# Kernel tuning notes

Hardware: AMD Instinct MI355X
Metric: run time of the kernel (lower is better)

Reference implementation:

```python
import jax, jax.numpy as jnp
import numpy as np

N_EMBD = 128
N_HEADS = 8
HEAD_SIZE = N_EMBD // N_HEADS  # 16
EPS = 1e-5


def _layernorm(x, g, b):
    m = jnp.mean(x, axis=-1, keepdims=True)
    v = jnp.mean(jnp.square(x - m), axis=-1, keepdims=True)
    return (x - m) * jax.lax.rsqrt(v + EPS) * g + b


def setup_inputs() -> dict:
    key = jax.random.key(0)
    ks = jax.random.split(key, 12)
    B, T, D, H, HS = 16, 1024, N_EMBD, N_HEADS, HEAD_SIZE
    s = 1.0 / np.sqrt(D)
    inp = {
        "x": jax.random.normal(ks[0], (B, T, D), jnp.float32),
        # per-head QKV projections (stacked over heads; matches ModuleList of Linear(D, HS))
        "Wq": jax.random.uniform(ks[1], (H, D, HS), jnp.float32, -s, s),
        "bq": jnp.zeros((H, HS), jnp.float32),
        "Wk": jax.random.uniform(ks[2], (H, D, HS), jnp.float32, -s, s),
        "bk": jnp.zeros((H, HS), jnp.float32),
        "Wv": jax.random.uniform(ks[3], (H, D, HS), jnp.float32, -s, s),
        "bv": jnp.zeros((H, HS), jnp.float32),
        "Wp": jax.random.uniform(ks[4], (H * HS, D), jnp.float32, -s, s),
        "bp": jnp.zeros((D,), jnp.float32),
        "W1": jax.random.uniform(ks[5], (D, 4 * D), jnp.float32, -s, s),
        "b1": jnp.zeros((4 * D,), jnp.float32),
        "W2": jax.random.uniform(ks[6], (4 * D, D), jnp.float32, -1.0 / np.sqrt(4 * D), 1.0 / np.sqrt(4 * D)),
        "b2": jnp.zeros((D,), jnp.float32),
        "g1": jnp.ones((D,), jnp.float32),
        "be1": jnp.zeros((D,), jnp.float32),
        "g2": jnp.ones((D,), jnp.float32),
        "be2": jnp.zeros((D,), jnp.float32),
    }
    return inp


def reference(x, Wq, bq, Wk, bk, Wv, bv, Wp, bp, W1, b1, W2, b2, g1, be1, g2, be2):
    B, T, D = x.shape
    # batched per-head projections: [B,T,D] x [H,D,HS] -> [B,H,T,HS]
    q = jnp.einsum("btd,hds->bhts", x, Wq) + bq[None, :, None, :]
    k = jnp.einsum("btd,hds->bhts", x, Wk) + bk[None, :, None, :]
    v = jnp.einsum("btd,hds->bhts", x, Wv) + bv[None, :, None, :]
    scores = jnp.einsum("bhts,bhus->bhtu", q, k) / np.sqrt(HEAD_SIZE).astype(np.float32)
    tril = jnp.tril(jnp.ones((T, T), x.dtype))
    # faithful to source: multiplicative + additive mask (not -inf where)
    scores = scores * tril - 1e12 * (1.0 - tril)
    attn = jax.nn.softmax(scores, axis=-1)
    out = jnp.einsum("bhtu,bhus->bhts", attn, v)  # [B,H,T,HS]
    # concat heads in head order -> [B,T,H*HS]
    out = out.transpose(0, 2, 1, 3).reshape(B, T, -1)
    attn_out = out @ Wp + bp
    x = _layernorm(attn_out + x, g1, be1)
    h = jax.nn.gelu(x @ W1 + b1, approximate=False) @ W2 + b2
    x = _layernorm(h + x, g2, be2)
    return x
```

## Files before the change

### kernel.cpp

```cpp
#include <hip/hip_runtime.h>
#include <hip/hip_bf16.h>
#include <math.h>

constexpr int NB  = 16;
constexpr int NT  = 1024;
constexpr int ND  = 128;
constexpr int NH  = 8;
constexpr int NHS = 16;
constexpr int NDH = 512;
constexpr long NBT = (long)NB * NT;

typedef __attribute__((ext_vector_type(8))) short short8;
typedef __attribute__((ext_vector_type(4))) float f32x4;
typedef __attribute__((ext_vector_type(16))) float f32x16;
typedef __attribute__((ext_vector_type(4))) unsigned short us4;

__device__ __forceinline__ unsigned short f2bf(float f) {
    __hip_bfloat16 h = __float2bfloat16(f);
    return *(unsigned short*)&h;
}

__device__ __forceinline__ short8 cvt8(const float* p) {
    const float4 f0 = *(const float4*)p;
    const float4 f1 = *(const float4*)(p + 4);
    union { short8 s; __hip_bfloat162 h[4]; } u;
    u.h[0] = __float22bfloat162_rn(make_float2(f0.x, f0.y));
    u.h[1] = __float22bfloat162_rn(make_float2(f0.z, f0.w));
    u.h[2] = __float22bfloat162_rn(make_float2(f1.x, f1.y));
    u.h[3] = __float22bfloat162_rn(make_float2(f1.z, f1.w));
    return u.s;
}

__device__ __forceinline__ float fast_gelu(float y) {
    const float t = y * y;
    const float u = __builtin_fmaf(y * 0.044715f, t, y);
    const float e = __builtin_amdgcn_exp2f(u * -2.302118131f);
    return y * __builtin_amdgcn_rcpf(1.0f + e);
}

__global__ __launch_bounds__(256) void k_prep(
    const float* __restrict__ Wq, const float* __restrict__ Wk,
    const float* __restrict__ Wv, __hip_bfloat16* __restrict__ Wqkvt)
{
    const int blk = blockIdx.x, tid = threadIdx.x;
    const int i0 = blk * 1024 + tid * 4;
    const int n = i0 >> 7, d0 = i0 & 127;
    const int sec = n >> 7, m = n & 127;
    const float* W = (sec == 0) ? Wq : (sec == 1) ? Wk : Wv;
    const float* src = W + (m >> 4) * 2048 + (m & 15);
    us4 v;
    #pragma unroll
    for (int j = 0; j < 4; ++j) v[j] = f2bf(src[(d0 + j) * 16]);
    *(us4*)((unsigned short*)Wqkvt + i0) = v;
}

__global__ __launch_bounds__(256) void k_qkv(
    const float* __restrict__ x, const __hip_bfloat16* __restrict__ Wqkvt,
    const float* __restrict__ bq, const float* __restrict__ bk,
    const float* __restrict__ bv,
    const float* __restrict__ Wp, const float* __restrict__ W1,
    const float* __restrict__ W2,
    __hip_bfloat16* __restrict__ Wpt, __hip_bfloat16* __restrict__ W1t,
    __hip_bfloat16* __restrict__ W2t,
    __hip_bfloat16* __restrict__ qo, __hip_bfloat16* __restrict__ ko,
    __hip_bfloat16* __restrict__ vo)
{
    __shared__ __align__(16) unsigned short st[32 * 392];
    const int tid = threadIdx.x;

    if (blockIdx.x >= 512) {
        const int blk = blockIdx.x - 512 + 48;
        us4 v;
        if (blk < 64) {
            const int i0 = (blk - 48) * 1024 + tid * 4;
            const int n = i0 >> 7, d0 = i0 & 127;
            #pragma unroll
            for (int j = 0; j < 4; ++j) v[j] = f2bf(Wp[(d0 + j) * 128 + n]);
            *(us4*)((unsigned short*)Wpt + i0) = v;
        } else if (blk < 128) {
            const int i0 = (blk - 64) * 1024 + tid * 4;
            const int n = i0 >> 7, d0 = i0 & 127;
            #pragma unroll
            for (int j = 0; j < 4; ++j) v[j] = f2bf(W1[(d0 + j) * 512 + n]);
            *(us4*)((unsigned short*)W1t + i0) = v;
        } else {
            const int i0 = (blk - 128) * 1024 + tid * 4;
            const int n = i0 >> 9, k0 = i0 & 511;
            #pragma unroll
            for (int j = 0; j < 4; ++j) v[j] = f2bf(W2[(k0 + j) * 128 + n]);
            *(us4*)((unsigned short*)W2t + i0) = v;
        }
        return;
    }

    const int w    = tid >> 6;
    const int lane = tid & 63;
    const int sL   = lane & 15;
    const int quad = lane >> 4;
    const int tok0 = blockIdx.x * 32;

    const unsigned short* W = (const unsigned short*)Wqkvt;

    short8 bx[2][4];
    #pragma unroll
    for (int tt = 0; tt < 2; ++tt)
        #pragma unroll
        for (int ks = 0; ks < 4; ++ks)
            bx[tt][ks] = cvt8(x + (size_t)(tok0 + tt * 16 + sL) * 128 + ks * 32 + quad * 8);

    f32x4 acc[6][2];
    #pragma unroll
    for (int ci = 0; ci < 6; ++ci)
        #pragma unroll
        for (int tt = 0; tt < 2; ++tt)
            acc[ci][tt] = (f32x4){0.f, 0.f, 0.f, 0.f};

    #pragma unroll
    for (int ks = 0; ks < 4; ++ks) {
        short8 aW[6];
        #pragma unroll
        for (int ci = 0; ci < 6; ++ci) {
            const int ct = w * 6 + ci;
            aW[ci] = *(const short8*)(W + (size_t)(ct * 16 + sL) * 128 + ks * 32 + quad * 8);
        }
        #pragma unroll
        for (int ci = 0; ci < 6; ++ci)
            #pragma unroll
            for (int tt = 0; tt < 2; ++tt)
                acc[ci][tt] = __builtin_amdgcn_mfma_f32_16x16x32_bf16(aW[ci], bx[tt][ks], acc[ci][tt], 0, 0, 0);
    }

    const float qscale = 0.3606737602f;
    #pragma unroll
    for (int ci = 0; ci < 6; ++ci) {
        const int ct = w * 6 + ci;
        const int kind = ct >> 3;
        const int ncc = (ct & 7) * 16 + quad * 4;
        const float4 bb = *(const float4*)(((kind == 0) ? bq : (kind == 1) ? bk : bv) + ncc);
        #pragma unroll
        for (int tt = 0; tt < 2; ++tt) {
            us4 v;
            #pragma unroll
            for (int r = 0; r < 4; ++r) {
                float val = acc[ci][tt][r] + ((const float*)&bb)[r];
                if (kind == 0) val *= qscale;
                v[r] = f2bf(val);
            }
            *(us4*)(st + (tt * 16 + sL) * 392 + ct * 16 + quad * 4) = v;
        }
    }
    __syncthreads();

    const int b = tok0 >> 10, tt0 = tok0 & 1023;
    {
        const int h = tid >> 5, tok = tid & 31;
        const unsigned short* sq = st + tok * 392 + h * 16;
        const unsigned short* sk = st + tok * 392 + 128 + h * 16;
        unsigned short* dq = (unsigned short*)qo + ((size_t)(b * 8 + h) * 1024 + tt0 + tok) * 16;
        unsigned short* dk = (unsigned short*)ko + ((size_t)(b * 8 + h) * 1024 + tt0 + tok) * 16;
        *(short8*)dq       = *(const short8*)sq;
        *(short8*)(dq + 8) = *(const short8*)(sq + 8);
        *(short8*)dk       = *(const short8*)sk;
        *(short8*)(dk + 8) = *(const short8*)(sk + 8);
    }
    if (tid < 128) {
        const int h = tid >> 4, s = tid & 15;
        unsigned short tmp[32];
        #pragma unroll
        for (int tok = 0; tok < 32; ++tok)
            tmp[tok] = st[tok * 392 + 256 + h * 16 + s];
        unsigned short* dv = (unsigned short*)vo + ((size_t)(b * 8 + h) * 16 + s) * 1024 + tt0;
        #pragma unroll
        for (int j = 0; j < 4; ++j)
            *(short8*)(dv + j * 8) = *(const short8*)(tmp + j * 8);
    }
}

__global__ __launch_bounds__(256) void k_attn(
    const __hip_bfloat16* __restrict__ qb, const __hip_bfloat16* __restrict__ kb,
    const __hip_bfloat16* __restrict__ vtb, __hip_bfloat16* __restrict__ att)
{
    __shared__ __align__(16) float stg[4][32 * 16];
    const int bh   = blockIdx.x & 127;
    const int sub  = blockIdx.x >> 7;
    const int wave = threadIdx.x >> 6;
    const int lane = threadIdx.x & 63;
    const int col  = lane & 31;
    const int hi   = lane >> 5;
    const int b = bh >> 3, h = bh & 7;
    const int tile = sub * 4 + wave;
    const int t0 = tile * 32;

    const unsigned short* qp = (const unsigned short*)qb  + (size_t)bh * NT * NHS;
    const unsigned short* kp = (const unsigned short*)kb  + (size_t)bh * NT * NHS;
    const unsigned short* vp = (const unsigned short*)vtb + (size_t)bh * NHS * NT;

    const short8 bQ = *(const short8*)(qp + (size_t)(t0 + col) * NHS + hi * 8);
    const unsigned short* vrow = vp + (size_t)(col & 15) * NT + hi * 8;

    f32x16 o;
    #pragma unroll
    for (int r = 0; r < 16; ++r) o[r] = 0.f;
    f32x16 zc;
    #pragma unroll
    for (int r = 0; r < 16; ++r) zc[r] = 0.f;
    float lp0 = 0.f, lp1 = 0.f, lp2 = 0.f, lp3 = 0.f;

    for (int c = 0; c <= tile; ++c) {
        const int u0 = c * 32;
        const short8 aK  = *(const short8*)(kp + (size_t)(u0 + col) * NHS + hi * 8);
        const short8 bV0 = *(const short8*)(vrow + u0);
        const short8 bV1 = *(const short8*)(vrow + u0 + 16);

        const f32x16 sT = __builtin_amdgcn_mfma_f32_32x32x16_bf16(aK, bQ, zc, 0, 0, 0);

        float p[16];
        if (c < tile) {
            #pragma unroll
            for (int r = 0; r < 16; ++r) p[r] = __builtin_amdgcn_exp2f(sT[r]);
        } else {
            const int kh = 4 * hi;
            #pragma unroll
            for (int r = 0; r < 16; ++r) {
                const int kc = (r & 3) + 8 * (r >> 2) + kh;
                const float e = __builtin_amdgcn_exp2f(sT[r]);
                p[r] = (kc <= col) ? e : 0.f;
            }
        }
        #pragma unroll
        for (int r = 0; r < 16; r += 4) {
            lp0 += p[r]; lp1 += p[r + 1]; lp2 += p[r + 2]; lp3 += p[r + 3];
        }

        int d[8];
        #pragma unroll
        for (int i = 0; i < 8; ++i) {
            __hip_bfloat162 hh = __float22bfloat162_rn(make_float2(p[2 * i], p[2 * i + 1]));
            d[i] = *(int*)&hh;
        }
        auto s0 = __builtin_amdgcn_permlane32_swap(d[0], d[2], false, false);
        auto s1 = __builtin_amdgcn_permlane32_swap(d[1], d[3], false, false);
        auto s2 = __builtin_amdgcn_permlane32_swap(d[4], d[6], false, false);
        auto s3 = __builtin_amdgcn_permlane32_swap(d[5], d[7], false, false);
        union { int i[4]; short8 v; } A0, A1;
        A0.i[0] = s0[0]; A0.i[1] = s1[0]; A0.i[2] = s0[1]; A0.i[3] = s1[1];
        A1.i[0] = s2[0]; A1.i[1] = s3[0]; A1.i[2] = s2[1]; A1.i[3] = s3[1];

        o = __builtin_amdgcn_mfma_f32_32x32x16_bf16(A0.v, bV0, o, 0, 0, 0);
        o = __builtin_amdgcn_mfma_f32_32x32x16_bf16(A1.v, bV1, o, 0, 0, 0);
    }

    float lp = (lp0 + lp1) + (lp2 + lp3);
    lp += __shfl_xor(lp, 32);
    const float inv = 1.0f / lp;

    float* sp = stg[wave];
    if (col < 16) {
        #pragma unroll
        for (int r = 0; r < 16; ++r) {
            const int qr = (r & 3) + 8 * (r >> 2) + 4 * hi;
            sp[qr * 16 + col] = o[r];
        }
    }
    __syncthreads();
    const float invq = __shfl(inv, lane >> 1);
    const float* rp = sp + (lane >> 1) * 16 + (lane & 1) * 8;
    const float4 va = *(const float4*)rp;
    const float4 vb = *(const float4*)(rp + 4);
    union { short8 v; unsigned short u[8]; } res;
    res.u[0] = f2bf(va.x * invq); res.u[1] = f2bf(va.y * invq);
    res.u[2] = f2bf(va.z * invq); res.u[3] = f2bf(va.w * invq);
    res.u[4] = f2bf(vb.x * invq); res.u[5] = f2bf(vb.y * invq);
    res.u[6] = f2bf(vb.z * invq); res.u[7] = f2bf(vb.w * invq);
    unsigned short* dst = (unsigned short*)att +
        ((size_t)b * NT + t0 + (lane >> 1)) * ND + h * NHS + (lane & 1) * 8;
    *(short8*)dst = res.v;
}

__global__ __launch_bounds__(256) void k_tail(
    const __hip_bfloat16* __restrict__ attb, const __hip_bfloat16* __restrict__ Wpt,
    const __hip_bfloat16* __restrict__ W1t, const __hip_bfloat16* __restrict__ W2t,
    const float* __restrict__ x, const float* __restrict__ bp,
    const float* __restrict__ g1, const float* __restrict__ be1,
    const float* __restrict__ b1, const float* __restrict__ b2,
    const float* __restrict__ g2, const float* __restrict__ be2,
    float* __restrict__ out)
{
    __shared__ float ys[32][132];
    __shared__ __align__(16) unsigned short l1b[32 * 136];
    __shared__ __align__(16) unsigned short midb[32 * 528];
    const int w    = threadIdx.x >> 6;
    const int lane = threadIdx.x & 63;
    const int sL   = lane & 15;
    const int quad = lane >> 4;
    const int tok0 = blockIdx.x * 32;

    {
        const unsigned short* A = (const unsigned short*)attb;
        const unsigned short* W = (const unsigned short*)Wpt;
        short8 bfr[2][4];
        #pragma unroll
        for (int tt = 0; tt < 2; ++tt)
            #pragma unroll
            for (int ks = 0; ks < 4; ++ks)
                bfr[tt][ks] = *(const short8*)(A + (size_t)(tok0 + tt * 16 + sL) * 128 + ks * 32 + quad * 8);

        f32x4 acc[2][2];
        #pragma unroll
        for (int ci = 0; ci < 2; ++ci)
            #pragma unroll
            for (int tt = 0; tt < 2; ++tt)
                acc[ci][tt] = (f32x4){0.f, 0.f, 0.f, 0.f};

        #pragma unroll
        for (int ks = 0; ks < 4; ++ks) {
            short8 aW[2];
            #pragma unroll
            for (int ci = 0; ci < 2; ++ci)
                aW[ci] = *(const short8*)(W + (size_t)((w * 2 + ci) * 16 + sL) * 128 + ks * 32 + quad * 8);
            #pragma unroll
            for (int ci = 0; ci < 2; ++ci)
                #pragma unroll
                for (int tt = 0; tt < 2; ++tt)
                    acc[ci][tt] = __builtin_amdgcn_mfma_f32_16x16x32_bf16(aW[ci], bfr[tt][ks], acc[ci][tt], 0, 0, 0);
        }
        #pragma unroll
        for (int ci = 0; ci < 2; ++ci) {
            const int n0 = (w * 2 + ci) * 16 + quad * 4;
            const float4 bb = *(const float4*)(bp + n0);
            #pragma unroll
            for (int tt = 0; tt < 2; ++tt) {
                float4 v;
                v.x = acc[ci][tt][0] + bb.x; v.y = acc[ci][tt][1] + bb.y;
                v.z = acc[ci][tt][2] + bb.z; v.w = acc[ci][tt][3] + bb.w;
                *(float4*)(&ys[tt * 16 + sL][n0]) = v;
            }
        }
    }
    __syncthreads();

    const int tok = threadIdx.x >> 3;
    const int l8  = threadIdx.x & 7;
    const int c0  = l8 * 16;
    {
        float vals[16];
        float s = 0.f, s2 = 0.f;
        #pragma unroll
        for (int ch = 0; ch < 4; ++ch) {
            const float4 ly = *(const float4*)&ys[tok][c0 + ch * 4];
            const float4 gx = *(const float4*)(x + (size_t)(tok0 + tok) * 128 + c0 + ch * 4);
            vals[ch*4+0] = ly.x + gx.x; vals[ch*4+1] = ly.y + gx.y;
            vals[ch*4+2] = ly.z + gx.z; vals[ch*4+3] = ly.w + gx.w;
            #pragma unroll
            for (int j = 0; j < 4; ++j) { s += vals[ch*4+j]; s2 += vals[ch*4+j] * vals[ch*4+j]; }
        }
        #pragma unroll
        for (int off = 1; off <= 4; off <<= 1) {
            s  += __shfl_xor(s, off, 8);
            s2 += __shfl_xor(s2, off, 8);
        }
        const float mean = s * (1.0f / 128.0f);
        const float var  = s2 * (1.0f / 128.0f) - mean * mean;
        const float rstd = rsqrtf(var + 1e-5f);
        #pragma unroll
        for (int ch = 0; ch < 4; ++ch) {
            const float4 gg = *(const float4*)(g1 + c0 + ch * 4);
            const float4 bb = *(const float4*)(be1 + c0 + ch * 4);
            float ln0 = (vals[ch*4+0] - mean) * rstd * gg.x + bb.x;
            float ln1v = (vals[ch*4+1] - mean) * rstd * gg.y + bb.y;
            float ln2v = (vals[ch*4+2] - mean) * rstd * gg.z + bb.z;
            float ln3 = (vals[ch*4+3] - mean) * rstd * gg.w + bb.w;
            ys[tok][c0 + ch*4 + 0] = ln0;
            ys[tok][c0 + ch*4 + 1] = ln1v;
            ys[tok][c0 + ch*4 + 2] = ln2v;
            ys[tok][c0 + ch*4 + 3] = ln3;
            us4 lb;
            lb[0] = f2bf(ln0); lb[1] = f2bf(ln1v); lb[2] = f2bf(ln2v); lb[3] = f2bf(ln3);
            *(us4*)(l1b + tok * 136 + c0 + ch * 4) = lb;
        }
    }
    __syncthreads();

    {
        const unsigned short* W = (const unsigned short*)W1t;
        short8 bl[2][4];
        #pragma unroll
        for (int tt = 0; tt < 2; ++tt)
            #pragma unroll
            for (int ks = 0; ks < 4; ++ks)
                bl[tt][ks] = *(const short8*)(l1b + (tt * 16 + sL) * 136 + ks * 32 + quad * 8);

        f32x4 acc[8][2];
        #pragma unroll
        for (int ci = 0; ci < 8; ++ci)
            #pragma unroll
            for (int tt = 0; tt < 2; ++tt)
                acc[ci][tt] = (f32x4){0.f, 0.f, 0.f, 0.f};

        #pragma unroll
        for (int ks = 0; ks < 4; ++ks) {
            short8 aW[8];
            #pragma unroll
            for (int ci = 0; ci < 8; ++ci)
                aW[ci] = *(const short8*)(W + (size_t)((w * 8 + ci) * 16 + sL) * 128 + ks * 32 + quad * 8);
            #pragma unroll
            for (int ci = 0; ci < 8; ++ci)
                #pragma unroll
                for (int tt = 0; tt < 2; ++tt)
                    acc[ci][tt] = __builtin_amdgcn_mfma_f32_16x16x32_bf16(aW[ci], bl[tt][ks], acc[ci][tt], 0, 0, 0);
        }
        #pragma unroll
        for (int ci = 0; ci < 8; ++ci) {
            const int n0 = (w * 8 + ci) * 16 + quad * 4;
            const float4 bb = *(const float4*)(b1 + n0);
            #pragma unroll
            for (int tt = 0; tt < 2; ++tt) {
                us4 v;
                v[0] = f2bf(fast_gelu(acc[ci][tt][0] + bb.x));
                v[1] = f2bf(fast_gelu(acc[ci][tt][1] + bb.y));
                v[2] = f2bf(fast_gelu(acc[ci][tt][2] + bb.z));
                v[3] = f2bf(fast_gelu(acc[ci][tt][3] + bb.w));
                *(us4*)(midb + (tt * 16 + sL) * 528 + n0) = v;
            }
        }
    }
    __syncthreads();

    f32x4 acc2[2][2];
    #pragma unroll
    for (int ci = 0; ci < 2; ++ci)
        #pragma unroll
        for (int tt = 0; tt < 2; ++tt)
            acc2[ci][tt] = (f32x4){0.f, 0.f, 0.f, 0.f};
    {
        const unsigned short* W = (const unsigned short*)W2t;
        #pragma unroll
        for (int ks = 0; ks < 16; ++ks) {
            short8 bm0 = *(const short8*)(midb + (size_t)sL * 528 + ks * 32 + quad * 8);
            short8 bm1 = *(const short8*)(midb + (size_t)(16 + sL) * 528 + ks * 32 + quad * 8);
            short8 aW0 = *(const short8*)(W + (size_t)((w * 2) * 16 + sL) * 512 + ks * 32 + quad * 8);
            short8 aW1 = *(const short8*)(W + (size_t)((w * 2 + 1) * 16 + sL) * 512 + ks * 32 + quad * 8);
            acc2[0][0] = __builtin_amdgcn_mfma_f32_16x16x32_bf16(aW0, bm0, acc2[0][0], 0, 0, 0);
            acc2[0][1] = __builtin_amdgcn_mfma_f32_16x16x32_bf16(aW0, bm1, acc2[0][1], 0, 0, 0);
            acc2[1][0] = __builtin_amdgcn_mfma_f32_16x16x32_bf16(aW1, bm0, acc2[1][0], 0, 0, 0);
            acc2[1][1] = __builtin_amdgcn_mfma_f32_16x16x32_bf16(aW1, bm1, acc2[1][1], 0, 0, 0);
        }
    }
    __syncthreads();
    float* ys2 = (float*)midb;
    #pragma unroll
    for (int ci = 0; ci < 2; ++ci) {
        const int n0 = (w * 2 + ci) * 16 + quad * 4;
        const float4 bb = *(const float4*)(b2 + n0);
        #pragma unroll
        for (int tt = 0; tt < 2; ++tt) {
            float4 v;
            v.x = acc2[ci][tt][0] + bb.x; v.y = acc2[ci][tt][1] + bb.y;
            v.z = acc2[ci][tt][2] + bb.z; v.w = acc2[ci][tt][3] + bb.w;
            *(float4*)(ys2 + (tt * 16 + sL) * 132 + n0) = v;
        }
    }
    __syncthreads();

    {
        float vals[16];
        float s = 0.f, s2 = 0.f;
        #pragma unroll
        for (int ch = 0; ch < 4; ++ch) {
            const float4 ly = *(const float4*)(ys2 + tok * 132 + c0 + ch * 4);
            const float4 gx = *(const float4*)&ys[tok][c0 + ch * 4];
            vals[ch*4+0] = ly.x + gx.x; vals[ch*4+1] = ly.y + gx.y;
            vals[ch*4+2] = ly.z + gx.z; vals[ch*4+3] = ly.w + gx.w;
            #pragma unroll
            for (int j = 0; j < 4; ++j) { s += vals[ch*4+j]; s2 += vals[ch*4+j] * vals[ch*4+j]; }
        }
        #pragma unroll
        for (int off = 1; off <= 4; off <<= 1) {
            s  += __shfl_xor(s, off, 8);
            s2 += __shfl_xor(s2, off, 8);
        }
        const float mean = s * (1.0f / 128.0f);
        const float var  = s2 * (1.0f / 128.0f) - mean * mean;
        const float rstd = rsqrtf(var + 1e-5f);
        #pragma unroll
        for (int ch = 0; ch < 4; ++ch) {
            const float4 gg = *(const float4*)(g2 + c0 + ch * 4);
            const float4 bb = *(const float4*)(be2 + c0 + ch * 4);
            float4 ln;
            ln.x = (vals[ch*4+0] - mean) * rstd * gg.x + bb.x;
            ln.y = (vals[ch*4+1] - mean) * rstd * gg.y + bb.y;
            ln.z = (vals[ch*4+2] - mean) * rstd * gg.z + bb.z;
            ln.w = (vals[ch*4+3] - mean) * rstd * gg.w + bb.w;
            *(float4*)(out + (size_t)(tok0 + tok) * 128 + c0 + ch * 4) = ln;
        }
    }
}

extern "C" void kernel_launch(void* const* d_in, const int* in_sizes, int n_in,
                              void* d_out, int out_size, void* d_ws, size_t ws_size,
                              hipStream_t stream)
{
    (void)in_sizes; (void)n_in; (void)out_size; (void)ws_size;
    const float* x   = (const float*)d_in[0];
    const float* Wq  = (const float*)d_in[1];
    const float* bq  = (const float*)d_in[2];
    const float* Wk  = (const float*)d_in[3];
    const float* bk  = (const float*)d_in[4];
    const float* Wv  = (const float*)d_in[5];
    const float* bv  = (const float*)d_in[6];
    const float* Wp  = (const float*)d_in[7];
    const float* bp  = (const float*)d_in[8];
    const float* W1  = (const float*)d_in[9];
    const float* b1  = (const float*)d_in[10];
    const float* W2  = (const float*)d_in[11];
    const float* b2  = (const float*)d_in[12];
    const float* g1  = (const float*)d_in[13];
    const float* be1 = (const float*)d_in[14];
    const float* g2  = (const float*)d_in[15];
    const float* be2 = (const float*)d_in[16];
    float* out = (float*)d_out;

    char* wsb = (char*)d_ws;
    __hip_bfloat16* qb   = (__hip_bfloat16*)wsb;
    __hip_bfloat16* kb   = (__hip_bfloat16*)(wsb + (4u  << 20));
    __hip_bfloat16* vtb  = (__hip_bfloat16*)(wsb + (8u  << 20));
    __hip_bfloat16* attb = (__hip_bfloat16*)(wsb + (12u << 20));
    __hip_bfloat16* Wqkvt= (__hip_bfloat16*)(wsb + (16u << 20));
    __hip_bfloat16* Wpt  = (__hip_bfloat16*)(wsb + (16u << 20) + (96u  << 10));
    __hip_bfloat16* W1t  = (__hip_bfloat16*)(wsb + (16u << 20) + (128u << 10));
    __hip_bfloat16* W2t  = (__hip_bfloat16*)(wsb + (16u << 20) + (256u << 10));

    k_prep<<<48,   256, 0, stream>>>(Wq, Wk, Wv, Wqkvt);
    k_qkv <<<656,  256, 0, stream>>>(x, Wqkvt, bq, bk, bv, Wp, W1, W2,
                                     Wpt, W1t, W2t, qb, kb, vtb);
    k_attn<<<1024, 256, 0, stream>>>(qb, kb, vtb, attb);
    k_tail<<<512,  256, 0, stream>>>(attb, Wpt, W1t, W2t, x, bp, g1, be1,
                                     b1, b2, g2, be2, out);
}
```

Before: 160.0 us.

## Fuse all stages into one persistent kernel with global atomic barriers

Merges the weight prep, QKV projection, causal attention and MLP tail into a single 512-block persistent kernel. The stages are separated by spin-wait grid barriers on atomic counters that are cleared with a memset before each launch. Each block now handles two attention tiles, pairing sub and 7-sub so that causal work is balanced across blocks. This removes three kernel launches and their inter-kernel gaps, at the cost of barrier spin overhead, a launch bound of 2 blocks per CU, and a risk of deadlock if not all blocks are co-resident.

```diff
diff --git a/kernel.cpp b/kernel.cpp
--- a/kernel.cpp
+++ b/kernel.cpp
@@ -9,6 +9,7 @@
 constexpr int NHS = 16;
 constexpr int NDH = 512;
 constexpr long NBT = (long)NB * NT;
+constexpr unsigned NBLK = 512;
 
 typedef __attribute__((ext_vector_type(8))) short short8;
 typedef __attribute__((ext_vector_type(4))) float f32x4;
@@ -38,460 +39,467 @@
     return y * __builtin_amdgcn_rcpf(1.0f + e);
 }
 
-__global__ __launch_bounds__(256) void k_prep(
-    const float* __restrict__ Wq, const float* __restrict__ Wk,
-    const float* __restrict__ Wv, __hip_bfloat16* __restrict__ Wqkvt)
+__device__ __forceinline__ void gbar(unsigned* ctr) {
+    __syncthreads();
+    if (threadIdx.x == 0) {
+        __threadfence();
+        atomicAdd(ctr, 1u);
+        int fuel = 50000000;
+        while (__hip_atomic_load(ctr, __ATOMIC_RELAXED, __HIP_MEMORY_SCOPE_AGENT) < NBLK
+               && --fuel > 0) {
+            __builtin_amdgcn_s_sleep(16);
+        }
+        __threadfence();
+    }
+    __syncthreads();
+}
+
+__global__ __launch_bounds__(256, 2) void k_fused(
+    const float* __restrict__ x,
+    const float* __restrict__ Wq, const float* __restrict__ bq,
+    const float* __restrict__ Wk, const float* __restrict__ bk,
+    const float* __restrict__ Wv, const float* __restrict__ bv,
+    const float* __restrict__ Wp, const float* __restrict__ bp,
+    const float* __restrict__ W1, const float* __restrict__ b1,
+    const float* __restrict__ W2, const float* __restrict__ b2,
+    const float* __restrict__ g1, const float* __restrict__ be1,
+    const float* __restrict__ g2, const float* __restrict__ be2,
+    __hip_bfloat16* __restrict__ Wqkvt, __hip_bfloat16* __restrict__ Wpt,
+    __hip_bfloat16* __restrict__ W1t,  __hip_bfloat16* __restrict__ W2t,
+    __hip_bfloat16* __restrict__ qb,   __hip_bfloat16* __restrict__ kb,
+    __hip_bfloat16* __restrict__ vtb,  __hip_bfloat16* __restrict__ attb,
+    unsigned* __restrict__ bars,
+    float* __restrict__ out)
 {
-    const int blk = blockIdx.x, tid = threadIdx.x;
-    const int i0 = blk * 1024 + tid * 4;
-    const int n = i0 >> 7, d0 = i0 & 127;
-    const int sec = n >> 7, m = n & 127;
-    const float* W = (sec == 0) ? Wq : (sec == 1) ? Wk : Wv;
-    const float* src = W + (m >> 4) * 2048 + (m & 15);
-    us4 v;
-    #pragma unroll
-    for (int j = 0; j < 4; ++j) v[j] = f2bf(src[(d0 + j) * 16]);
-    *(us4*)((unsigned short*)Wqkvt + i0) = v;
-}
-
-__global__ __launch_bounds__(256) void k_qkv(
-    const float* __restrict__ x, const __hip_bfloat16* __restrict__ Wqkvt,
-    const float* __restrict__ bq, const float* __restrict__ bk,
-    const float* __restrict__ bv,
-    const float* __restrict__ Wp, const float* __restrict__ W1,
-    const float* __restrict__ W2,
-    __hip_bfloat16* __restrict__ Wpt, __hip_bfloat16* __restrict__ W1t,
-    __hip_bfloat16* __restrict__ W2t,
-    __hip_bfloat16* __restrict__ qo, __hip_bfloat16* __restrict__ ko,
-    __hip_bfloat16* __restrict__ vo)
-{
-    __shared__ __align__(16) unsigned short st[32 * 392];
-    const int tid = threadIdx.x;
-
-    if (blockIdx.x >= 512) {
-        const int blk = blockIdx.x - 512 + 48;
-        us4 v;
-        if (blk < 64) {
-            const int i0 = (blk - 48) * 1024 + tid * 4;
-            const int n = i0 >> 7, d0 = i0 & 127;
-            #pragma unroll
-            for (int j = 0; j < 4; ++j) v[j] = f2bf(Wp[(d0 + j) * 128 + n]);
-            *(us4*)((unsigned short*)Wpt + i0) = v;
-        } else if (blk < 128) {
-            const int i0 = (blk - 64) * 1024 + tid * 4;
-            const int n = i0 >> 7, d0 = i0 & 127;
-            #pragma unroll
-            for (int j = 0; j < 4; ++j) v[j] = f2bf(W1[(d0 + j) * 512 + n]);
-            *(us4*)((unsigned short*)W1t + i0) = v;
-        } else {
-            const int i0 = (blk - 128) * 1024 + tid * 4;
-            const int n = i0 >> 9, k0 = i0 & 511;
-            #pragma unroll
-            for (int j = 0; j < 4; ++j) v[j] = f2bf(W2[(k0 + j) * 128 + n]);
-            *(us4*)((unsigned short*)W2t + i0) = v;
-        }
-        return;
-    }
-
+    __shared__ __align__(16) char smem[59392];
+    const int bid  = blockIdx.x;
+    const int tid  = threadIdx.x;
     const int w    = tid >> 6;
     const int lane = tid & 63;
     const int sL   = lane & 15;
     const int quad = lane >> 4;
-    const int tok0 = blockIdx.x * 32;
-
-    const unsigned short* W = (const unsigned short*)Wqkvt;
-
-    short8 bx[2][4];
-    #pragma unroll
-    for (int tt = 0; tt < 2; ++tt)
-        #pragma unroll
-        for (int ks = 0; ks < 4; ++ks)
-            bx[tt][ks] = cvt8(x + (size_t)(tok0 + tt * 16 + sL) * 128 + ks * 32 + quad * 8);
-
-    f32x4 acc[6][2];
-    #pragma unroll
-    for (int ci = 0; ci < 6; ++ci)
+
+    if (bid < 192) {
+        us4 v;
+        if (bid < 48) {
+            const int i0 = bid * 1024 + tid * 4;
+            const int n = i0 >> 7, d0 = i0 & 127;
+            const int sec = n >> 7, m = n & 127;
+            const float* W = (sec == 0) ? Wq : (sec == 1) ? Wk : Wv;
+            const float* src = W + (m >> 4) * 2048 + (m & 15);
+            #pragma unroll
+            for (int j = 0; j < 4; ++j) v[j] = f2bf(src[(d0 + j) * 16]);
+            *(us4*)((unsigned short*)Wqkvt + i0) = v;
+        } else if (bid < 64) {
+            const int i0 = (bid - 48) * 1024 + tid * 4;
+            const int n = i0 >> 7, d0 = i0 & 127;
+            #pragma unroll
+            for (int j = 0; j < 4; ++j) v[j] = f2bf(Wp[(d0 + j) * 128 + n]);
+            *(us4*)((unsigned short*)Wpt + i0) = v;
+        } else if (bid < 128) {
+            const int i0 = (bid - 64) * 1024 + tid * 4;
+            const int n = i0 >> 7, d0 = i0 & 127;
+            #pragma unroll
+            for (int j = 0; j < 4; ++j) v[j] = f2bf(W1[(d0 + j) * 512 + n]);
+            *(us4*)((unsigned short*)W1t + i0) = v;
+        } else {
+            const int i0 = (bid - 128) * 1024 + tid * 4;
+            const int n = i0 >> 9, k0 = i0 & 511;
+            #pragma unroll
+            for (int j = 0; j < 4; ++j) v[j] = f2bf(W2[(k0 + j) * 128 + n]);
+            *(us4*)((unsigned short*)W2t + i0) = v;
+        }
+    }
+    gbar(bars + 0);
+
+    {
+        unsigned short* st = (unsigned short*)smem;
+        const int tok0 = bid * 32;
+        const unsigned short* W = (const unsigned short*)Wqkvt;
+
+        short8 bx[2][4];
         #pragma unroll
         for (int tt = 0; tt < 2; ++tt)
-            acc[ci][tt] = (f32x4){0.f, 0.f, 0.f, 0.f};
-
-    #pragma unroll
-    for (int ks = 0; ks < 4; ++ks) {
-        short8 aW[6];
+            #pragma unroll
+            for (int ks = 0; ks < 4; ++ks)
+                bx[tt][ks] = cvt8(x + (size_t)(tok0 + tt * 16 + sL) * 128 + ks * 32 + quad * 8);
+
+        f32x4 acc[6][2];
+        #pragma unroll
+        for (int ci = 0; ci < 6; ++ci)
+            #pragma unroll
+            for (int tt = 0; tt < 2; ++tt)
+                acc[ci][tt] = (f32x4){0.f, 0.f, 0.f, 0.f};
+
+        #pragma unroll
+        for (int ks = 0; ks < 4; ++ks) {
+            short8 aW[6];
+            #pragma unroll
+            for (int ci = 0; ci < 6; ++ci) {
+                const int ct = w * 6 + ci;
+                aW[ci] = *(const short8*)(W + (size_t)(ct * 16 + sL) * 128 + ks * 32 + quad * 8);
+            }
+            #pragma unroll
+            for (int ci = 0; ci < 6; ++ci)
+                #pragma unroll
+                for (int tt = 0; tt < 2; ++tt)
+                    acc[ci][tt] = __builtin_amdgcn_mfma_f32_16x16x32_bf16(aW[ci], bx[tt][ks], acc[ci][tt], 0, 0, 0);
+        }
+
+        const float qscale = 0.3606737602f;
         #pragma unroll
         for (int ci = 0; ci < 6; ++ci) {
             const int ct = w * 6 + ci;
-            aW[ci] = *(const short8*)(W + (size_t)(ct * 16 + sL) * 128 + ks * 32 + quad * 8);
-        }
-        #pragma unroll
-        for (int ci = 0; ci < 6; ++ci)
+            const int kind = ct >> 3;
+            const int ncc = (ct & 7) * 16 + quad * 4;
+            const float4 bb = *(const float4*)(((kind == 0) ? bq : (kind == 1) ? bk : bv) + ncc);
+            #pragma unroll
+            for (int tt = 0; tt < 2; ++tt) {
+                us4 v;
+                #pragma unroll
+                for (int r = 0; r < 4; ++r) {
+                    float val = acc[ci][tt][r] + ((const float*)&bb)[r];
+                    if (kind == 0) val *= qscale;
+                    v[r] = f2bf(val);
+                }
+                *(us4*)(st + (tt * 16 + sL) * 392 + ct * 16 + quad * 4) = v;
+            }
+        }
+        __syncthreads();
+
+        const int b = tok0 >> 10, tt0 = tok0 & 1023;
+        {
+            const int h = tid >> 5, tok = tid & 31;
+            const unsigned short* sq = st + tok * 392 + h * 16;
+            const unsigned short* sk = st + tok * 392 + 128 + h * 16;
+            unsigned short* dq = (unsigned short*)qb + ((size_t)(b * 8 + h) * 1024 + tt0 + tok) * 16;
+            unsigned short* dk = (unsigned short*)kb + ((size_t)(b * 8 + h) * 1024 + tt0 + tok) * 16;
+            *(short8*)dq       = *(const short8*)sq;
+            *(short8*)(dq + 8) = *(const short8*)(sq + 8);
+            *(short8*)dk       = *(const short8*)sk;
+            *(short8*)(dk + 8) = *(const short8*)(sk + 8);
+        }
+        if (tid < 128) {
+            const int h = tid >> 4, s = tid & 15;
+            unsigned short tmp[32];
+            #pragma unroll
+            for (int tok = 0; tok < 32; ++tok)
+                tmp[tok] = st[tok * 392 + 256 + h * 16 + s];
+            unsigned short* dv = (unsigned short*)vtb + ((size_t)(b * 8 + h) * 16 + s) * 1024 + tt0;
+            #pragma unroll
+            for (int j = 0; j < 4; ++j)
+                *(short8*)(dv + j * 8) = *(const short8*)(tmp + j * 8);
+        }
+    }
+    gbar(bars + 16);
+
+    {
+        float* sp = (float*)smem + w * 512;
+        const int col = lane & 31;
+        const int hi  = lane >> 5;
+        const int bh = bid & 127;
+        const int spair = bid >> 7;
+        const int b = bh >> 3, h = bh & 7;
+
+        const unsigned short* qp = (const unsigned short*)qb  + (size_t)bh * NT * NHS;
+        const unsigned short* kp = (const unsigned short*)kb  + (size_t)bh * NT * NHS;
+        const unsigned short* vp = (const unsigned short*)vtb + (size_t)bh * NHS * NT;
+        const unsigned short* vrow = vp + (size_t)(col & 15) * NT + hi * 8;
+
+        f32x16 zc;
+        #pragma unroll
+        for (int r = 0; r < 16; ++r) zc[r] = 0.f;
+
+        #pragma unroll 1
+        for (int ui = 0; ui < 2; ++ui) {
+            const int sub  = ui ? (7 - spair) : spair;
+            const int tile = sub * 4 + w;
+            const int t0 = tile * 32;
+
+            const short8 bQ = *(const short8*)(qp + (size_t)(t0 + col) * NHS + hi * 8);
+
+            f32x16 o;
+            #pragma unroll
+            for (int r = 0; r < 16; ++r) o[r] = 0.f;
+            float lp0 = 0.f, lp1 = 0.f, lp2 = 0.f, lp3 = 0.f;
+
+            for (int c = 0; c <= tile; ++c) {
+                const int u0 = c * 32;
+                const short8 aK  = *(const short8*)(kp + (size_t)(u0 + col) * NHS + hi * 8);
+                const short8 bV0 = *(const short8*)(vrow + u0);
+                const short8 bV1 = *(const short8*)(vrow + u0 + 16);
+
+                const f32x16 sT = __builtin_amdgcn_mfma_f32_32x32x16_bf16(aK, bQ, zc, 0, 0, 0);
+
+                float p[16];
+                if (c < tile) {
+                    #pragma unroll
+                    for (int r = 0; r < 16; ++r) p[r] = __builtin_amdgcn_exp2f(sT[r]);
+                } else {
+                    const int kh = 4 * hi;
+                    #pragma unroll
+                    for (int r = 0; r < 16; ++r) {
+                        const int kc = (r & 3) + 8 * (r >> 2) + kh;
+                        const float e = __builtin_amdgcn_exp2f(sT[r]);
+                        p[r] = (kc <= col) ? e : 0.f;
+                    }
+                }
+                #pragma unroll
+                for (int r = 0; r < 16; r += 4) {
+                    lp0 += p[r]; lp1 += p[r + 1]; lp2 += p[r + 2]; lp3 += p[r + 3];
+                }
+
+                int d[8];
+                #pragma unroll
+                for (int i = 0; i < 8; ++i) {
+                    __hip_bfloat162 hh = __float22bfloat162_rn(make_float2(p[2 * i], p[2 * i + 1]));
+                    d[i] = *(int*)&hh;
+                }
+                auto s0 = __builtin_amdgcn_permlane32_swap(d[0], d[2], false, false);
+                auto s1 = __builtin_amdgcn_permlane32_swap(d[1], d[3], false, false);
+                auto s2 = __builtin_amdgcn_permlane32_swap(d[4], d[6], false, false);
+                auto s3 = __builtin_amdgcn_permlane32_swap(d[5], d[7], false, false);
+                union { int i[4]; short8 v; } A0, A1;
+                A0.i[0] = s0[0]; A0.i[1] = s1[0]; A0.i[2] = s0[1]; A0.i[3] = s1[1];
+                A1.i[0] = s2[0]; A1.i[1] = s3[0]; A1.i[2] = s2[1]; A1.i[3] = s3[1];
+
+                o = __builtin_amdgcn_mfma_f32_32x32x16_bf16(A0.v, bV0, o, 0, 0, 0);
+                o = __builtin_amdgcn_mfma_f32_32x32x16_bf16(A1.v, bV1, o, 0, 0, 0);
+            }
+
+            float lp = (lp0 + lp1) + (lp2 + lp3);
+            lp += __shfl_xor(lp, 32);
+            const float inv = 1.0f / lp;
+
+            if (col < 16) {
+                #pragma unroll
+                for (int r = 0; r < 16; ++r) {
+                    const int qr = (r & 3) + 8 * (r >> 2) + 4 * hi;
+                    sp[qr * 16 + col] = o[r];
+                }
+            }
+            __syncthreads();
+            const float invq = __shfl(inv, lane >> 1);
+            const float* rp = sp + (lane >> 1) * 16 + (lane & 1) * 8;
+            const float4 va = *(const float4*)rp;
+            const float4 vb = *(const float4*)(rp + 4);
+            union { short8 v; unsigned short u[8]; } res;
+            res.u[0] = f2bf(va.x * invq); res.u[1] = f2bf(va.y * invq);
+            res.u[2] = f2bf(va.z * invq); res.u[3] = f2bf(va.w * invq);
+            res.u[4] = f2bf(vb.x * invq); res.u[5] = f2bf(vb.y * invq);
+            res.u[6] = f2bf(vb.z * invq); res.u[7] = f2bf(vb.w * invq);
+            unsigned short* dst = (unsigned short*)attb +
+                ((size_t)b * NT + t0 + (lane >> 1)) * ND + h * NHS + (lane & 1) * 8;
+            *(short8*)dst = res.v;
+            __syncthreads();
+        }
+    }
+    gbar(bars + 32);
+
+    {
+        float (*ys)[132]    = (float(*)[132])smem;
+        unsigned short* l1b = (unsigned short*)(smem + 16896);
+        unsigned short* midb= (unsigned short*)(smem + 16896 + 8704);
+        const int tok0 = bid * 32;
+
+        {
+            const unsigned short* A = (const unsigned short*)attb;
+            const unsigned short* W = (const unsigned short*)Wpt;
+            short8 bfr[2][4];
             #pragma unroll
             for (int tt = 0; tt < 2; ++tt)
-                acc[ci][tt] = __builtin_amdgcn_mfma_f32_16x16x32_bf16(aW[ci], bx[tt][ks], acc[ci][tt], 0, 0, 0);
-    }
-
-    const float qscale = 0.3606737602f;
-    #pragma unroll
-    for (int ci = 0; ci < 6; ++ci) {
-        const int ct = w * 6 + ci;
-        const int kind = ct >> 3;
-        const int ncc = (ct & 7) * 16 + quad * 4;
-        const float4 bb = *(const float4*)(((kind == 0) ? bq : (kind == 1) ? bk : bv) + ncc);
-        #pragma unroll
-        for (int tt = 0; tt < 2; ++tt) {
-            us4 v;
-            #pragma unroll
-            for (int r = 0; r < 4; ++r) {
-                float val = acc[ci][tt][r] + ((const float*)&bb)[r];
-                if (kind == 0) val *= qscale;
-                v[r] = f2bf(val);
-            }
-            *(us4*)(st + (tt * 16 + sL) * 392 + ct * 16 + quad * 4) = v;
-        }
-    }
-    __syncthreads();
-
-    const int b = tok0 >> 10, tt0 = tok0 & 1023;
-    {
-        const int h = tid >> 5, tok = tid & 31;
-        const unsigned short* sq = st + tok * 392 + h * 16;
-        const unsigned short* sk = st + tok * 392 + 128 + h * 16;
-        unsigned short* dq = (unsigned short*)qo + ((size_t)(b * 8 + h) * 1024 + tt0 + tok) * 16;
-        unsigned short* dk = (unsigned short*)ko + ((size_t)(b * 8 + h) * 1024 + tt0 + tok) * 16;
-        *(short8*)dq       = *(const short8*)sq;
-        *(short8*)(dq + 8) = *(const short8*)(sq + 8);
-        *(short8*)dk       = *(const short8*)sk;
-        *(short8*)(dk + 8) = *(const short8*)(sk + 8);
-    }
-    if (tid < 128) {
-        const int h = tid >> 4, s = tid & 15;
-        unsigned short tmp[32];
-        #pragma unroll
-        for (int tok = 0; tok < 32; ++tok)
-            tmp[tok] = st[tok * 392 + 256 + h * 16 + s];
-        unsigned short* dv = (unsigned short*)vo + ((size_t)(b * 8 + h) * 16 + s) * 1024 + tt0;
-        #pragma unroll
-        for (int j = 0; j < 4; ++j)
-            *(short8*)(dv + j * 8) = *(const short8*)(tmp + j * 8);
-    }
-}
-
-__global__ __launch_bounds__(256) void k_attn(
-    const __hip_bfloat16* __restrict__ qb, const __hip_bfloat16* __restrict__ kb,
-    const __hip_bfloat16* __restrict__ vtb, __hip_bfloat16* __restrict__ att)
-{
-    __shared__ __align__(16) float stg[4][32 * 16];
-    const int bh   = blockIdx.x & 127;
-    const int sub  = blockIdx.x >> 7;
-    const int wave = threadIdx.x >> 6;
-    const int lane = threadIdx.x & 63;
-    const int col  = lane & 31;
-    const int hi   = lane >> 5;
-    const int b = bh >> 3, h = bh & 7;
-    const int tile = sub * 4 + wave;
-    const int t0 = tile * 32;
-
-    const unsigned short* qp = (const unsigned short*)qb  + (size_t)bh * NT * NHS;
-    const unsigned short* kp = (const unsigned short*)kb  + (size_t)bh * NT * NHS;
-    const unsigned short* vp = (const unsigned short*)vtb + (size_t)bh * NHS * NT;
-
-    const short8 bQ = *(const short8*)(qp + (size_t)(t0 + col) * NHS + hi * 8);
-    const unsigned short* vrow = vp + (size_t)(col & 15) * NT + hi * 8;
-
-    f32x16 o;
-    #pragma unroll
-    for (int r = 0; r < 16; ++r) o[r] = 0.f;
-    f32x16 zc;
-    #pragma unroll
-    for (int r = 0; r < 16; ++r) zc[r] = 0.f;
-    float lp0 = 0.f, lp1 = 0.f, lp2 = 0.f, lp3 = 0.f;
-
-    for (int c = 0; c <= tile; ++c) {
-        const int u0 = c * 32;
-        const short8 aK  = *(const short8*)(kp + (size_t)(u0 + col) * NHS + hi * 8);
-        const short8 bV0 = *(const short8*)(vrow + u0);
-        const short8 bV1 = *(const short8*)(vrow + u0 + 16);
-
-        const f32x16 sT = __builtin_amdgcn_mfma_f32_32x32x16_bf16(aK, bQ, zc, 0, 0, 0);
-
-        float p[16];
-        if (c < tile) {
-            #pragma unroll
-            for (int r = 0; r < 16; ++r) p[r] = __builtin_amdgcn_exp2f(sT[r]);
-        } else {
-            const int kh = 4 * hi;
-            #pragma unroll
-            for (int r = 0; r < 16; ++r) {
-                const int kc = (r & 3) + 8 * (r >> 2) + kh;
-                const float e = __builtin_amdgcn_exp2f(sT[r]);
-                p[r] = (kc <= col) ? e : 0.f;
-            }
-        }
-        #pragma unroll
-        for (int r = 0; r < 16; r += 4) {
-            lp0 += p[r]; lp1 += p[r + 1]; lp2 += p[r + 2]; lp3 += p[r + 3];
-        }
-
-        int d[8];
-        #pragma unroll
-        for (int i = 0; i < 8; ++i) {
-            __hip_bfloat162 hh = __float22bfloat162_rn(make_float2(p[2 * i], p[2 * i + 1]));
-            d[i] = *(int*)&hh;
-        }
-        auto s0 = __builtin_amdgcn_permlane32_swap(d[0], d[2], false, false);
-        auto s1 = __builtin_amdgcn_permlane32_swap(d[1], d[3], false, false);
-        auto s2 = __builtin_amdgcn_permlane32_swap(d[4], d[6], false, false);
-        auto s3 = __builtin_amdgcn_permlane32_swap(d[5], d[7], false, false);
-        union { int i[4]; short8 v; } A0, A1;
-        A0.i[0] = s0[0]; A0.i[1] = s1[0]; A0.i[2] = s0[1]; A0.i[3] = s1[1];
-        A1.i[0] = s2[0]; A1.i[1] = s3[0]; A1.i[2] = s2[1]; A1.i[3] = s3[1];
-
-        o = __builtin_amdgcn_mfma_f32_32x32x16_bf16(A0.v, bV0, o, 0, 0, 0);
-        o = __builtin_amdgcn_mfma_f32_32x32x16_bf16(A1.v, bV1, o, 0, 0, 0);
-    }
-
-    float lp = (lp0 + lp1) + (lp2 + lp3);
-    lp += __shfl_xor(lp, 32);
-    const float inv = 1.0f / lp;
-
-    float* sp = stg[wave];
-    if (col < 16) {
-        #pragma unroll
-        for (int r = 0; r < 16; ++r) {
-            const int qr = (r & 3) + 8 * (r >> 2) + 4 * hi;
-            sp[qr * 16 + col] = o[r];
-        }
-    }
-    __syncthreads();
-    const float invq = __shfl(inv, lane >> 1);
-    const float* rp = sp + (lane >> 1) * 16 + (lane & 1) * 8;
-    const float4 va = *(const float4*)rp;
-    const float4 vb = *(const float4*)(rp + 4);
-    union { short8 v; unsigned short u[8]; } res;
-    res.u[0] = f2bf(va.x * invq); res.u[1] = f2bf(va.y * invq);
-    res.u[2] = f2bf(va.z * invq); res.u[3] = f2bf(va.w * invq);
-    res.u[4] = f2bf(vb.x * invq); res.u[5] = f2bf(vb.y * invq);
-    res.u[6] = f2bf(vb.z * invq); res.u[7] = f2bf(vb.w * invq);
-    unsigned short* dst = (unsigned short*)att +
-        ((size_t)b * NT + t0 + (lane >> 1)) * ND + h * NHS + (lane & 1) * 8;
-    *(short8*)dst = res.v;
-}
-
-__global__ __launch_bounds__(256) void k_tail(
-    const __hip_bfloat16* __restrict__ attb, const __hip_bfloat16* __restrict__ Wpt,
-    const __hip_bfloat16* __restrict__ W1t, const __hip_bfloat16* __restrict__ W2t,
-    const float* __restrict__ x, const float* __restrict__ bp,
-    const float* __restrict__ g1, const float* __restrict__ be1,
-    const float* __restrict__ b1, const float* __restrict__ b2,
-    const float* __restrict__ g2, const float* __restrict__ be2,
-    float* __restrict__ out)
-{
-    __shared__ float ys[32][132];
-    __shared__ __align__(16) unsigned short l1b[32 * 136];
-    __shared__ __align__(16) unsigned short midb[32 * 528];
-    const int w    = threadIdx.x >> 6;
-    const int lane = threadIdx.x & 63;
-    const int sL   = lane & 15;
-    const int quad = lane >> 4;
-    const int tok0 = blockIdx.x * 32;
-
-    {
-        const unsigned short* A = (const unsigned short*)attb;
-        const unsigned short* W = (const unsigned short*)Wpt;
-        short8 bfr[2][4];
-        #pragma unroll
-        for (int tt = 0; tt < 2; ++tt)
-            #pragma unroll
-            for (int ks = 0; ks < 4; ++ks)
-                bfr[tt][ks] = *(const short8*)(A + (size_t)(tok0 + tt * 16 + sL) * 128 + ks * 32 + quad * 8);
-
-        f32x4 acc[2][2];
+                #pragma unroll
+                for (int ks = 0; ks < 4; ++ks)
+                    bfr[tt][ks] = *(const short8*)(A + (size_t)(tok0 + tt * 16 + sL) * 128 + ks * 32 + quad * 8);
+
+            f32x4 acc[2][2];
+            #pragma unroll
+            for (int ci = 0; ci < 2; ++ci)
+                #pragma unroll
+                for (int tt = 0; tt < 2; ++tt)
+                    acc[ci][tt] = (f32x4){0.f, 0.f, 0.f, 0.f};
+
+            #pragma unroll
+            for (int ks = 0; ks < 4; ++ks) {
+                short8 aW[2];
+                #pragma unroll
+                for (int ci = 0; ci < 2; ++ci)
+                    aW[ci] = *(const short8*)(W + (size_t)((w * 2 + ci) * 16 + sL) * 128 + ks * 32 + quad * 8);
+                #pragma unroll
+                for (int ci = 0; ci < 2; ++ci)
+                    #pragma unroll
+                    for (int tt = 0; tt < 2; ++tt)
+                        acc[ci][tt] = __builtin_amdgcn_mfma_f32_16x16x32_bf16(aW[ci], bfr[tt][ks], acc[ci][tt], 0, 0, 0);
+            }
+            #pragma unroll
+            for (int ci = 0; ci < 2; ++ci) {
+                const int n0 = (w * 2 + ci) * 16 + quad * 4;
+                const float4 bb = *(const float4*)(bp + n0);
+                #pragma unroll
+                for (int tt = 0; tt < 2; ++tt) {
+                    float4 v;
+                    v.x = acc[ci][tt][0] + bb.x; v.y = acc[ci][tt][1] + bb.y;
+                    v.z = acc[ci][tt][2] + bb.z; v.w = acc[ci][tt][3] + bb.w;
+                    *(float4*)(&ys[tt * 16 + sL][n0]) = v;
+                }
+            }
+        }
+        __syncthreads();
+
+        const int tok = tid >> 3;
+        const int l8  = tid & 7;
+        const int c0  = l8 * 16;
+        {
+            float vals[16];
+            float s = 0.f, s2 = 0.f;
+            #pragma unroll
+            for (int ch = 0; ch < 4; ++ch) {
+                const float4 ly = *(const float4*)&ys[tok][c0 + ch * 4];
+                const float4 gx = *(const float4*)(x + (size_t)(tok0 + tok) * 128 + c0 + ch * 4);
+                vals[ch*4+0] = ly.x + gx.x; vals[ch*4+1] = ly.y + gx.y;
+                vals[ch*4+2] = ly.z + gx.z; vals[ch*4+3] = ly.w + gx.w;
+                #pragma unroll
+                for (int j = 0; j < 4; ++j) { s += vals[ch*4+j]; s2 += vals[ch*4+j] * vals[ch*4+j]; }
+            }
+            #pragma unroll
+            for (int off = 1; off <= 4; off <<= 1) {
+                s  += __shfl_xor(s, off, 8);
+                s2 += __shfl_xor(s2, off, 8);
+            }
+            const float mean = s * (1.0f / 128.0f);
+            const float var  = s2 * (1.0f / 128.0f) - mean * mean;
+            const float rstd = rsqrtf(var + 1e-5f);
+            #pragma unroll
+            for (int ch = 0; ch < 4; ++ch) {
+                const float4 gg = *(const float4*)(g1 + c0 + ch * 4);
+                const float4 bb = *(const float4*)(be1 + c0 + ch * 4);
+                float ln0 = (vals[ch*4+0] - mean) * rstd * gg.x + bb.x;
+                float ln1v = (vals[ch*4+1] - mean) * rstd * gg.y + bb.y;
+                float ln2v = (vals[ch*4+2] - mean) * rstd * gg.z + bb.z;
+                float ln3 = (vals[ch*4+3] - mean) * rstd * gg.w + bb.w;
+                ys[tok][c0 + ch*4 + 0] = ln0;
+                ys[tok][c0 + ch*4 + 1] = ln1v;
+                ys[tok][c0 + ch*4 + 2] = ln2v;
+                ys[tok][c0 + ch*4 + 3] = ln3;
+                us4 lb;
+                lb[0] = f2bf(ln0); lb[1] = f2bf(ln1v); lb[2] = f2bf(ln2v); lb[3] = f2bf(ln3);
+                *(us4*)(l1b + tok * 136 + c0 + ch * 4) = lb;
+            }
+        }
+        __syncthreads();
+
+        {
+            const unsigned short* W = (const unsigned short*)W1t;
+            short8 bl[2][4];
+            #pragma unroll
+            for (int tt = 0; tt < 2; ++tt)
+                #pragma unroll
+                for (int ks = 0; ks < 4; ++ks)
+                    bl[tt][ks] = *(const short8*)(l1b + (tt * 16 + sL) * 136 + ks * 32 + quad * 8);
+
+            f32x4 acc[8][2];
+            #pragma unroll
+            for (int ci = 0; ci < 8; ++ci)
+                #pragma unroll
+                for (int tt = 0; tt < 2; ++tt)
+                    acc[ci][tt] = (f32x4){0.f, 0.f, 0.f, 0.f};
+
+            #pragma unroll
+            for (int ks = 0; ks < 4; ++ks) {
+                short8 aW[8];
+                #pragma unroll
+                for (int ci = 0; ci < 8; ++ci)
+                    aW[ci] = *(const short8*)(W + (size_t)((w * 8 + ci) * 16 + sL) * 128 + ks * 32 + quad * 8);
+                #pragma unroll
+                for (int ci = 0; ci < 8; ++ci)
+                    #pragma unroll
+                    for (int tt = 0; tt < 2; ++tt)
+                        acc[ci][tt] = __builtin_amdgcn_mfma_f32_16x16x32_bf16(aW[ci], bl[tt][ks], acc[ci][tt], 0, 0, 0);
+            }
+            #pragma unroll
+            for (int ci = 0; ci < 8; ++ci) {
+                const int n0 = (w * 8 + ci) * 16 + quad * 4;
+                const float4 bb = *(const float4*)(b1 + n0);
+                #pragma unroll
+                for (int tt = 0; tt < 2; ++tt) {
+                    us4 v;
+                    v[0] = f2bf(fast_gelu(acc[ci][tt][0] + bb.x));
+                    v[1] = f2bf(fast_gelu(acc[ci][tt][1] + bb.y));
+                    v[2] = f2bf(fast_gelu(acc[ci][tt][2] + bb.z));
+                    v[3] = f2bf(fast_gelu(acc[ci][tt][3] + bb.w));
+                    *(us4*)(midb + (tt * 16 + sL) * 528 + n0) = v;
+                }
+            }
+        }
+        __syncthreads();
+
+        f32x4 acc2[2][2];
         #pragma unroll
         for (int ci = 0; ci < 2; ++ci)
             #pragma unroll
             for (int tt = 0; tt < 2; ++tt)
-                acc[ci][tt] = (f32x4){0.f, 0.f, 0.f, 0.f};
-
-        #pragma unroll
-        for (int ks = 0; ks < 4; ++ks) {
-            short8 aW[2];
-            #pragma unroll
-            for (int ci = 0; ci < 2; ++ci)
-                aW[ci] = *(const short8*)(W + (size_t)((w * 2 + ci) * 16 + sL) * 128 + ks * 32 + quad * 8);
-            #pragma unroll
-            for (int ci = 0; ci < 2; ++ci)
-                #pragma unroll
-                for (int tt = 0; tt < 2; ++tt)
-                    acc[ci][tt] = __builtin_amdgcn_mfma_f32_16x16x32_bf16(aW[ci], bfr[tt][ks], acc[ci][tt], 0, 0, 0);
-        }
+                acc2[ci][tt] = (f32x4){0.f, 0.f, 0.f, 0.f};
+        {
+            const unsigned short* W = (const unsigned short*)W2t;
+            #pragma unroll
+            for (int ks = 0; ks < 16; ++ks) {
+                short8 bm0 = *(const short8*)(midb + (size_t)sL * 528 + ks * 32 + quad * 8);
+                short8 bm1 = *(const short8*)(midb + (size_t)(16 + sL) * 528 + ks * 32 + quad * 8);
+                short8 aW0 = *(const short8*)(W + (size_t)((w * 2) * 16 + sL) * 512 + ks * 32 + quad * 8);
+                short8 aW1 = *(const short8*)(W + (size_t)((w * 2 + 1) * 16 + sL) * 512 + ks * 32 + quad * 8);
+                acc2[0][0] = __builtin_amdgcn_mfma_f32_16x16x32_bf16(aW0, bm0, acc2[0][0], 0, 0, 0);
+                acc2[0][1] = __builtin_amdgcn_mfma_f32_16x16x32_bf16(aW0, bm1, acc2[0][1], 0, 0, 0);
+                acc2[1][0] = __builtin_amdgcn_mfma_f32_16x16x32_bf16(aW1, bm0, acc2[1][0], 0, 0, 0);
+                acc2[1][1] = __builtin_amdgcn_mfma_f32_16x16x32_bf16(aW1, bm1, acc2[1][1], 0, 0, 0);
+            }
+        }
+        __syncthreads();
+        float* ys2 = (float*)midb;
         #pragma unroll
         for (int ci = 0; ci < 2; ++ci) {
             const int n0 = (w * 2 + ci) * 16 + quad * 4;
-            const float4 bb = *(const float4*)(bp + n0);
+            const float4 bb = *(const float4*)(b2 + n0);
             #pragma unroll
             for (int tt = 0; tt < 2; ++tt) {
                 float4 v;
-                v.x = acc[ci][tt][0] + bb.x; v.y = acc[ci][tt][1] + bb.y;
-                v.z = acc[ci][tt][2] + bb.z; v.w = acc[ci][tt][3] + bb.w;
-                *(float4*)(&ys[tt * 16 + sL][n0]) = v;
-            }
-        }
-    }
-    __syncthreads();
-
-    const int tok = threadIdx.x >> 3;
-    const int l8  = threadIdx.x & 7;
-    const int c0  = l8 * 16;
-    {
-        float vals[16];
-        float s = 0.f, s2 = 0.f;
-        #pragma unroll
-        for (int ch = 0; ch < 4; ++ch) {
-            const float4 ly = *(const float4*)&ys[tok][c0 + ch * 4];
-            const float4 gx = *(const float4*)(x + (size_t)(tok0 + tok) * 128 + c0 + ch * 4);
-            vals[ch*4+0] = ly.x + gx.x; vals[ch*4+1] = ly.y + gx.y;
-            vals[ch*4+2] = ly.z + gx.z; vals[ch*4+3] = ly.w + gx.w;
-            #pragma unroll
-            for (int j = 0; j < 4; ++j) { s += vals[ch*4+j]; s2 += vals[ch*4+j] * vals[ch*4+j]; }
-        }
-        #pragma unroll
-        for (int off = 1; off <= 4; off <<= 1) {
-            s  += __shfl_xor(s, off, 8);
-            s2 += __shfl_xor(s2, off, 8);
-        }
-        const float mean = s * (1.0f / 128.0f);
-        const float var  = s2 * (1.0f / 128.0f) - mean * mean;
-        const float rstd = rsqrtf(var + 1e-5f);
-        #pragma unroll
-        for (int ch = 0; ch < 4; ++ch) {
-            const float4 gg = *(const float4*)(g1 + c0 + ch * 4);
-            const float4 bb = *(const float4*)(be1 + c0 + ch * 4);
-            float ln0 = (vals[ch*4+0] - mean) * rstd * gg.x + bb.x;
-            float ln1v = (vals[ch*4+1] - mean) * rstd * gg.y + bb.y;
-            float ln2v = (vals[ch*4+2] - mean) * rstd * gg.z + bb.z;
-            float ln3 = (vals[ch*4+3] - mean) * rstd * gg.w + bb.w;
-            ys[tok][c0 + ch*4 + 0] = ln0;
-            ys[tok][c0 + ch*4 + 1] = ln1v;
-            ys[tok][c0 + ch*4 + 2] = ln2v;
-            ys[tok][c0 + ch*4 + 3] = ln3;
-            us4 lb;
-            lb[0] = f2bf(ln0); lb[1] = f2bf(ln1v); lb[2] = f2bf(ln2v); lb[3] = f2bf(ln3);
-            *(us4*)(l1b + tok * 136 + c0 + ch * 4) = lb;
-        }
-    }
-    __syncthreads();
-
-    {
-        const unsigned short* W = (const unsigned short*)W1t;
-        short8 bl[2][4];
-        #pragma unroll
-        for (int tt = 0; tt < 2; ++tt)
-            #pragma unroll
-            for (int ks = 0; ks < 4; ++ks)
-                bl[tt][ks] = *(const short8*)(l1b + (tt * 16 + sL) * 136 + ks * 32 + quad * 8);
-
-        f32x4 acc[8][2];
-        #pragma unroll
-        for (int ci = 0; ci < 8; ++ci)
-            #pragma unroll
-            for (int tt = 0; tt < 2; ++tt)
-                acc[ci][tt] = (f32x4){0.f, 0.f, 0.f, 0.f};
-
-        #pragma unroll
-        for (int ks = 0; ks < 4; ++ks) {
-            short8 aW[8];
-            #pragma unroll
-            for (int ci = 0; ci < 8; ++ci)
-                aW[ci] = *(const short8*)(W + (size_t)((w * 8 + ci) * 16 + sL) * 128 + ks * 32 + quad * 8);
-            #pragma unroll
-            for (int ci = 0; ci < 8; ++ci)
-                #pragma unroll
-                for (int tt = 0; tt < 2; ++tt)
-                    acc[ci][tt] = __builtin_amdgcn_mfma_f32_16x16x32_bf16(aW[ci], bl[tt][ks], acc[ci][tt], 0, 0, 0);
-        }
-        #pragma unroll
-        for (int ci = 0; ci < 8; ++ci) {
-            const int n0 = (w * 8 + ci) * 16 + quad * 4;
-            const float4 bb = *(const float4*)(b1 + n0);
-            #pragma unroll
-            for (int tt = 0; tt < 2; ++tt) {
-                us4 v;
-                v[0] = f2bf(fast_gelu(acc[ci][tt][0] + bb.x));
-                v[1] = f2bf(fast_gelu(acc[ci][tt][1] + bb.y));
-                v[2] = f2bf(fast_gelu(acc[ci][tt][2] + bb.z));
-                v[3] = f2bf(fast_gelu(acc[ci][tt][3] + bb.w));
-                *(us4*)(midb + (tt * 16 + sL) * 528 + n0) = v;
-            }
-        }
-    }
-    __syncthreads();
-
-    f32x4 acc2[2][2];
-    #pragma unroll
-    for (int ci = 0; ci < 2; ++ci)
-        #pragma unroll
-        for (int tt = 0; tt < 2; ++tt)
-            acc2[ci][tt] = (f32x4){0.f, 0.f, 0.f, 0.f};
-    {
-        const unsigned short* W = (const unsigned short*)W2t;
-        #pragma unroll
-        for (int ks = 0; ks < 16; ++ks) {
-            short8 bm0 = *(const short8*)(midb + (size_t)sL * 528 + ks * 32 + quad * 8);
-            short8 bm1 = *(const short8*)(midb + (size_t)(16 + sL) * 528 + ks * 32 + quad * 8);
-            short8 aW0 = *(const short8*)(W + (size_t)((w * 2) * 16 + sL) * 512 + ks * 32 + quad * 8);
-            short8 aW1 = *(const short8*)(W + (size_t)((w * 2 + 1) * 16 + sL) * 512 + ks * 32 + quad * 8);
-            acc2[0][0] = __builtin_amdgcn_mfma_f32_16x16x32_bf16(aW0, bm0, acc2[0][0], 0, 0, 0);
-            acc2[0][1] = __builtin_amdgcn_mfma_f32_16x16x32_bf16(aW0, bm1, acc2[0][1], 0, 0, 0);
-            acc2[1][0] = __builtin_amdgcn_mfma_f32_16x16x32_bf16(aW1, bm0, acc2[1][0], 0, 0, 0);
-            acc2[1][1] = __builtin_amdgcn_mfma_f32_16x16x32_bf16(aW1, bm1, acc2[1][1], 0, 0, 0);
-        }
-    }
-    __syncthreads();
-    float* ys2 = (float*)midb;
-    #pragma unroll
-    for (int ci = 0; ci < 2; ++ci) {
-        const int n0 = (w * 2 + ci) * 16 + quad * 4;
-        const float4 bb = *(const float4*)(b2 + n0);
-        #pragma unroll
-        for (int tt = 0; tt < 2; ++tt) {
-            float4 v;
-            v.x = acc2[ci][tt][0] + bb.x; v.y = acc2[ci][tt][1] + bb.y;
-            v.z = acc2[ci][tt][2] + bb.z; v.w = acc2[ci][tt][3] + bb.w;
-            *(float4*)(ys2 + (tt * 16 + sL) * 132 + n0) = v;
-        }
-    }
-    __syncthreads();
-
-    {
-        float vals[16];
-        float s = 0.f, s2 = 0.f;
-        #pragma unroll
-        for (int ch = 0; ch < 4; ++ch) {
-            const float4 ly = *(const float4*)(ys2 + tok * 132 + c0 + ch * 4);
-            const float4 gx = *(const float4*)&ys[tok][c0 + ch * 4];
-            vals[ch*4+0] = ly.x + gx.x; vals[ch*4+1] = ly.y + gx.y;
-            vals[ch*4+2] = ly.z + gx.z; vals[ch*4+3] = ly.w + gx.w;
-            #pragma unroll
-            for (int j = 0; j < 4; ++j) { s += vals[ch*4+j]; s2 += vals[ch*4+j] * vals[ch*4+j]; }
-        }
-        #pragma unroll
-        for (int off = 1; off <= 4; off <<= 1) {
-            s  += __shfl_xor(s, off, 8);
-            s2 += __shfl_xor(s2, off, 8);
-        }
-        const float mean = s * (1.0f / 128.0f);
-        const float var  = s2 * (1.0f / 128.0f) - mean * mean;
-        const float rstd = rsqrtf(var + 1e-5f);
-        #pragma unroll
-        for (int ch = 0; ch < 4; ++ch) {
-            const float4 gg = *(const float4*)(g2 + c0 + ch * 4);
-            const float4 bb = *(const float4*)(be2 + c0 + ch * 4);
-            float4 ln;
-            ln.x = (vals[ch*4+0] - mean) * rstd * gg.x + bb.x;
-            ln.y = (vals[ch*4+1] - mean) * rstd * gg.y + bb.y;
-            ln.z = (vals[ch*4+2] - mean) * rstd * gg.z + bb.z;
-            ln.w = (vals[ch*4+3] - mean) * rstd * gg.w + bb.w;
-            *(float4*)(out + (size_t)(tok0 + tok) * 128 + c0 + ch * 4) = ln;
+                v.x = acc2[ci][tt][0] + bb.x; v.y = acc2[ci][tt][1] + bb.y;
+                v.z = acc2[ci][tt][2] + bb.z; v.w = acc2[ci][tt][3] + bb.w;
+                *(float4*)(ys2 + (tt * 16 + sL) * 132 + n0) = v;
+            }
+        }
+        __syncthreads();
+
+        {
+            float vals[16];
+            float s = 0.f, s2 = 0.f;
+            #pragma unroll
+            for (int ch = 0; ch < 4; ++ch) {
+                const float4 ly = *(const float4*)(ys2 + tok * 132 + c0 + ch * 4);
+                const float4 gx = *(const float4*)&ys[tok][c0 + ch * 4];
+                vals[ch*4+0] = ly.x + gx.x; vals[ch*4+1] = ly.y + gx.y;
+                vals[ch*4+2] = ly.z + gx.z; vals[ch*4+3] = ly.w + gx.w;
+                #pragma unroll
+                for (int j = 0; j < 4; ++j) { s += vals[ch*4+j]; s2 += vals[ch*4+j] * vals[ch*4+j]; }
+            }
+            #pragma unroll
+            for (int off = 1; off <= 4; off <<= 1) {
+                s  += __shfl_xor(s, off, 8);
+                s2 += __shfl_xor(s2, off, 8);
+            }
+            const float mean = s * (1.0f / 128.0f);
+            const float var  = s2 * (1.0f / 128.0f) - mean * mean;
+            const float rstd = rsqrtf(var + 1e-5f);
+            #pragma unroll
+            for (int ch = 0; ch < 4; ++ch) {
+                const float4 gg = *(const float4*)(g2 + c0 + ch * 4);
+                const float4 bb = *(const float4*)(be2 + c0 + ch * 4);
+                float4 ln;
+                ln.x = (vals[ch*4+0] - mean) * rstd * gg.x + bb.x;
+                ln.y = (vals[ch*4+1] - mean) * rstd * gg.y + bb.y;
+                ln.z = (vals[ch*4+2] - mean) * rstd * gg.z + bb.z;
+                ln.w = (vals[ch*4+3] - mean) * rstd * gg.w + bb.w;
+                *(float4*)(out + (size_t)(tok0 + tok) * 128 + c0 + ch * 4) = ln;
+            }
         }
     }
 }
@@ -529,11 +537,11 @@
     __hip_bfloat16* Wpt  = (__hip_bfloat16*)(wsb + (16u << 20) + (96u  << 10));
     __hip_bfloat16* W1t  = (__hip_bfloat16*)(wsb + (16u << 20) + (128u << 10));
     __hip_bfloat16* W2t  = (__hip_bfloat16*)(wsb + (16u << 20) + (256u << 10));
-
-    k_prep<<<48,   256, 0, stream>>>(Wq, Wk, Wv, Wqkvt);
-    k_qkv <<<656,  256, 0, stream>>>(x, Wqkvt, bq, bk, bv, Wp, W1, W2,
-                                     Wpt, W1t, W2t, qb, kb, vtb);
-    k_attn<<<1024, 256, 0, stream>>>(qb, kb, vtb, attb);
-    k_tail<<<512,  256, 0, stream>>>(attb, Wpt, W1t, W2t, x, bp, g1, be1,
-                                     b1, b2, g2, be2, out);
+    unsigned* bars       = (unsigned*)(wsb + (16u << 20) + (512u << 10));
+
+    hipMemsetAsync(bars, 0, 256, stream);
+    k_fused<<<NBLK, 256, 0, stream>>>(
+        x, Wq, bq, Wk, bk, Wv, bv, Wp, bp, W1, b1, W2, b2,
+        g1, be1, g2, be2,
+        Wqkvt, Wpt, W1t, W2t, qb, kb, vtb, attb, bars, out);
 }
```

Measured after the change: 314.2 us. 96.4% more time.
